# Performance work log

Measured on AMD Instinct MI355X. Metric: run time of the kernel, lower is better.

## Reference

```python
import jax, jax.numpy as jnp
import numpy as np

OUT, IN, GROUP, RANK, NPROT, BATCH = 4096, 4096, 128, 32, 32, 4096


def setup_inputs() -> dict:
    key = jax.random.key(0)
    k = jax.random.split(key, 7)
    n = OUT * IN
    x = jax.random.normal(k[0], (BATCH, IN), dtype=jnp.float32)
    # two int4 values per byte; byte values in [0,256)
    packed_int4 = jax.random.randint(k[1], (n // 2,), 0, 256, dtype=jnp.int32)
    # positive per-group scales (typical int4 scale magnitudes)
    scales = jax.random.uniform(k[2], (IN // GROUP,), dtype=jnp.float32, minval=0.005, maxval=0.02)
    svd_u = jax.random.normal(k[3], (OUT, RANK), dtype=jnp.float32) * 0.01
    svd_v = jax.random.normal(k[4], (IN, RANK), dtype=jnp.float32) * 0.01
    protected_channels = jax.random.normal(k[5], (NPROT, IN), dtype=jnp.float32) * 0.02
    # unique protected row indices
    protected_indices = jax.random.permutation(k[6], OUT)[:NPROT].astype(jnp.int32)
    return {
        "x": x,
        "packed_int4": packed_int4,
        "scales": scales,
        "svd_u": svd_u,
        "svd_v": svd_v,
        "protected_channels": protected_channels,
        "protected_indices": protected_indices,
    }


def reference(x, packed_int4, scales, svd_u, svd_v, protected_channels, protected_indices):
    out_f = svd_u.shape[0]
    in_f = x.shape[-1]
    group = in_f // scales.shape[0]
    # Unpack: original puts low nibbles in first half of the flat array,
    # high nibbles in the second half (split layout, not interleaved).
    lo = packed_int4 & 15
    hi = (packed_int4 >> 4) & 15
    unpacked = jnp.concatenate([lo, hi])  # [out*in]
    w_quant = (unpacked.astype(jnp.float32) - 8.0).reshape(out_f, in_f)
    # per-group dequant over input columns
    w = (w_quant.reshape(out_f, -1, group) * scales[None, :, None]).reshape(out_f, in_f)
    # low-rank SVD correction
    w = w + svd_u @ svd_v.T
    # protected output channels overwrite full rows
    w = w.at[protected_indices].set(protected_channels)
    out = x @ w.T  # [batch, out]
    return out.astype(jnp.float16)
```

## Files before the change

kernel.cpp:

```cpp
#include <hip/hip_runtime.h>
#include <hip/hip_bf16.h>
#include <hip/hip_fp16.h>

#define OUT_F 4096
#define IN_F  4096
#define BATCH 4096
#define RANK  32
#define KPAD  4160
#define NKB   130
#define NT    65

typedef __hip_bfloat16 bf16;
using bf16x8 = __attribute__((ext_vector_type(8))) short;
using f32x4  = __attribute__((ext_vector_type(4))) float;


__device__ __forceinline__ void gload_lds16(const void* g, void* l) {
  __builtin_amdgcn_global_load_lds(
      (const __attribute__((address_space(1))) unsigned int*)g,
      (__attribute__((address_space(3))) unsigned int*)l,
      16, 0, 0);
}

__device__ __forceinline__ unsigned short bf16_bits(float f) {
  bf16 h = __float2bfloat16(f);
  return *(unsigned short*)&h;
}

#define SBAR() asm volatile("s_barrier" ::: "memory")

__global__ __launch_bounds__(256) void prep_misc(const float* __restrict__ v,
                                                 const float* __restrict__ scales,
                                                 const float* __restrict__ u,
                                                 const int* __restrict__ pidx,
                                                 bf16* __restrict__ vst,
                                                 bf16* __restrict__ B) {
  int bid = blockIdx.x;
  if (bid < 512) {
    int gid = bid * 256 + threadIdx.x;
    int c = gid >> 5, r = gid & 31;
    float val = v[(size_t)c * RANK + r] / scales[c >> 7];
    vst[(size_t)r * IN_F + c] = __float2bfloat16(val);
  } else {
    int i = (bid - 512) * 256 + threadIdx.x;
    int o = i >> 6, j = i & 63;
    float val = (j < RANK) ? u[o * RANK + j] : 0.f;
#pragma unroll
    for (int jj = 0; jj < 32; ++jj)
      if (pidx[jj] == o) val = 0.f;
    B[(size_t)o * KPAD + IN_F + j] = __float2bfloat16(val);
  }
}

__global__ __launch_bounds__(512) void prep_a(const float* __restrict__ x,
                                              const float* __restrict__ scales,
                                              const bf16* __restrict__ vst,
                                              bf16* __restrict__ A) {
  __shared__ __align__(16) char lds[16384];
  int rb = blockIdx.x;
  int tid = threadIdx.x, w = tid >> 6, l = tid & 63;

  for (int c = 0; c < 8; ++c) {
#pragma unroll
    for (int j = 0; j < 2; ++j) {
      int r = w * 2 + j;
      const float* xr = x + (size_t)(rb * 16 + r) * IN_F + c * 512 + l * 8;
      float sv = scales[(c * 512 + l * 8) >> 7];
      float4 v0 = *(const float4*)xr;
      float4 v1 = *(const float4*)(xr + 4);
      bf16x8 pk;
      pk[0] = (short)bf16_bits(v0.x * sv); pk[1] = (short)bf16_bits(v0.y * sv);
      pk[2] = (short)bf16_bits(v0.z * sv); pk[3] = (short)bf16_bits(v0.w * sv);
      pk[4] = (short)bf16_bits(v1.x * sv); pk[5] = (short)bf16_bits(v1.y * sv);
      pk[6] = (short)bf16_bits(v1.z * sv); pk[7] = (short)bf16_bits(v1.w * sv);
      int kb = l >> 2;
      int byte = kb * 1024 + (((l & 3) << 4) + r) * 16;
      *(bf16x8*)(lds + (byte ^ ((kb & 7) << 4))) = pk;
    }
    __syncthreads();
#pragma unroll
    for (int j = 0; j < 2; ++j) {
      int f = w * 2 + j;
      int byte = f * 1024 + l * 16;
      bf16x8 pk = *(const bf16x8*)(lds + (byte ^ ((f & 7) << 4)));
      *(bf16x8*)(A + ((size_t)rb * NKB + c * 16 + f) * 512 + (size_t)l * 8) = pk;
    }
    __syncthreads();
  }

  const bf16* abase = A + (size_t)rb * NKB * 512 + (size_t)l * 8;
  const bf16* brow0 = vst + (size_t)(l & 15) * IN_F + ((l >> 4) << 3);
  const bf16* brow1 = vst + (size_t)(16 + (l & 15)) * IN_F + ((l >> 4) << 3);
  f32x4 acc0 = (f32x4){0.f, 0.f, 0.f, 0.f};
  f32x4 acc1 = (f32x4){0.f, 0.f, 0.f, 0.f};
#pragma unroll 8
  for (int k32 = w * 16; k32 < w * 16 + 16; ++k32) {
    bf16x8 av  = *(const bf16x8*)(abase + (size_t)k32 * 512);
    bf16x8 bv0 = *(const bf16x8*)(brow0 + k32 * 32);
    bf16x8 bv1 = *(const bf16x8*)(brow1 + k32 * 32);
    acc0 = __builtin_amdgcn_mfma_f32_16x16x32_bf16(av, bv0, acc0, 0, 0, 0);
    acc1 = __builtin_amdgcn_mfma_f32_16x16x32_bf16(av, bv1, acc1, 0, 0, 0);
  }
  *(f32x4*)(lds + w * 2048 + l * 32)      = acc0;
  *(f32x4*)(lds + w * 2048 + l * 32 + 16) = acc1;
  __syncthreads();
  if (w == 1) {
    bf16x8 z = (bf16x8){0, 0, 0, 0, 0, 0, 0, 0};
    *(bf16x8*)(A + ((size_t)rb * NKB + 129) * 512 + (size_t)l * 8) = z;
  }
  if (w == 0) {
#pragma unroll
    for (int ww = 1; ww < 8; ++ww) {
      acc0 += *(const f32x4*)(lds + ww * 2048 + l * 32);
      acc1 += *(const f32x4*)(lds + ww * 2048 + l * 32 + 16);
    }
    bf16* base = A + ((size_t)rb * NKB + 128) * 512;
    int c0 = l & 15, c1 = 16 + (l & 15);
#pragma unroll
    for (int r = 0; r < 4; ++r) {
      int row15 = ((l >> 4) << 2) + r;
      base[(c0 >> 3) * 128 + row15 * 8 + (c0 & 7)] = __float2bfloat16(acc0[r]);
      base[(c1 >> 3) * 128 + row15 * 8 + (c1 & 7)] = __float2bfloat16(acc1[r]);
    }
  }
}

__global__ __launch_bounds__(256) void prep_b(const int* __restrict__ packed,
                                              const float* __restrict__ pc,
                                              const float* __restrict__ scales,
                                              const int* __restrict__ pidx,
                                              bf16* __restrict__ B) {
  size_t i = (size_t)blockIdx.x * 256 + threadIdx.x;
  int4 p = ((const int4*)packed)[i];
  size_t e = i * 4;
  int o = (int)(e >> 12);
  int c = (int)(e & 4095);
  int pi_lo = -1, pi_hi = -1;
#pragma unroll
  for (int j = 0; j < 32; ++j) {
    int pr = pidx[j];
    if (pr == o) pi_lo = j;
    if (pr == o + 2048) pi_hi = j;
  }
  int vals[4] = {p.x, p.y, p.z, p.w};
  unsigned short lo[4], hi[4];
#pragma unroll
  for (int j = 0; j < 4; ++j) {
    lo[j] = bf16_bits((float)((vals[j] & 15) - 8));
    hi[j] = bf16_bits((float)(((vals[j] >> 4) & 15) - 8));
  }
  if (pi_lo >= 0) {
    float sv = scales[c >> 7];
#pragma unroll
    for (int j = 0; j < 4; ++j)
      lo[j] = bf16_bits(pc[(size_t)pi_lo * IN_F + c + j] / sv);
  }
  if (pi_hi >= 0) {
    float sv = scales[c >> 7];
#pragma unroll
    for (int j = 0; j < 4; ++j)
      hi[j] = bf16_bits(pc[(size_t)pi_hi * IN_F + c + j] / sv);
  }
  *(ushort4*)(B + (size_t)o * KPAD + c) = make_ushort4(lo[0], lo[1], lo[2], lo[3]);
  *(ushort4*)(B + (size_t)(o + 2048) * KPAD + c) = make_ushort4(hi[0], hi[1], hi[2], hi[3]);
}

__global__ __launch_bounds__(512, 2) void gemm_bt(const bf16* __restrict__ A,
                                                  const bf16* __restrict__ B,
                                                  float* __restrict__ out) {
  __shared__ __align__(16) bf16 Bs[4 * 256 * 64];

  int bid = blockIdx.x;
  int swz = (bid & 7) * 32 + (bid >> 3);
  int brow = (swz >> 4) << 8;
  int bcol = (swz & 15) << 8;

  int tid = threadIdx.x;
  int lane = tid & 63;
  int wave = tid >> 6;
  int wr = wave >> 1;
  int wc = wave & 1;

  f32x4 acc[4][8];
#pragma unroll
  for (int m = 0; m < 4; ++m)
#pragma unroll
    for (int n = 0; n < 8; ++n)
      acc[m][n] = (f32x4){0.f, 0.f, 0.f, 0.f};

  const char* abase[4];
  int rbw = (brow >> 4) + wr * 4;
#pragma unroll
  for (int m = 0; m < 4; ++m)
    abase[m] = (const char*)A + ((size_t)(rbw + m) * NKB) * 1024 + lane * 16;

  int boff[8];
#pragma unroll
  for (int n = 0; n < 8; ++n) {
    int rbr = wc * 128 + n * 16 + (lane & 15);
    int s0 = (lane >> 4) ^ (rbr & 7);
    boff[n] = rbr * 128 + (s0 << 4);
  }

  const bf16* gB[4]; int lB[4];
#pragma unroll
  for (int q = 0; q < 4; ++q) {
    int idx = q * 512 + tid;
    int row = idx >> 3, slot = idx & 7;
    gB[q] = B + (size_t)(bcol + row) * KPAD + ((slot ^ (row & 7)) << 3);
    lB[q] = idx << 4;
  }
  char* bs0 = (char*)Bs;

  bf16x8 a0[4][2], a1[4][2];
#pragma unroll
  for (int m = 0; m < 4; ++m)
#pragma unroll
    for (int kk = 0; kk < 2; ++kk)
      a0[m][kk] = *(const bf16x8*)(abase[m] + kk * 1024);
#pragma unroll
  for (int kt = 0; kt < 3; ++kt)
#pragma unroll
    for (int q = 0; q < 4; ++q)
      gload_lds16(gB[q] + kt * 64, bs0 + kt * 32768 + lB[q]);
  asm volatile("s_waitcnt vmcnt(8)" ::: "memory");
  SBAR();

  auto tile_body = [&](int t, bf16x8 (&Au)[4][2], bf16x8 (&Ap)[4][2], bool pref) {
    const char* rb_ = bs0 + (t & 3) * 32768;
    char* wb = bs0 + ((t + 3) & 3) * 32768;
    int kt = (t + 3 < NT) ? (t + 3) : (NT - 1);
#pragma unroll
    for (int p = 0; p < 4; ++p) {
      if (p == 0 && pref) {
#pragma unroll
        for (int m = 0; m < 4; ++m)
#pragma unroll
          for (int kk = 0; kk < 2; ++kk)
            Ap[m][kk] = *(const bf16x8*)(abase[m] + (size_t)(2 * (t + 1) + kk) * 1024);
      }
      bf16x8 bv0k0 = *(const bf16x8*)(rb_ + boff[2 * p]);
      bf16x8 bv0k1 = *(const bf16x8*)(rb_ + (boff[2 * p] ^ 64));
      bf16x8 bv1k0 = *(const bf16x8*)(rb_ + boff[2 * p + 1]);
      bf16x8 bv1k1 = *(const bf16x8*)(rb_ + (boff[2 * p + 1] ^ 64));
      gload_lds16(gB[p] + (size_t)kt * 64, wb + lB[p]);
      __builtin_amdgcn_s_setprio(1);
#pragma unroll
      for (int m = 0; m < 4; ++m) {
        acc[m][2 * p]     = __builtin_amdgcn_mfma_f32_16x16x32_bf16(Au[m][0], bv0k0, acc[m][2 * p], 0, 0, 0);
        acc[m][2 * p]     = __builtin_amdgcn_mfma_f32_16x16x32_bf16(Au[m][1], bv0k1, acc[m][2 * p], 0, 0, 0);
        acc[m][2 * p + 1] = __builtin_amdgcn_mfma_f32_16x16x32_bf16(Au[m][0], bv1k0, acc[m][2 * p + 1], 0, 0, 0);
        acc[m][2 * p + 1] = __builtin_amdgcn_mfma_f32_16x16x32_bf16(Au[m][1], bv1k1, acc[m][2 * p + 1], 0, 0, 0);
      }
      __builtin_amdgcn_s_setprio(0);
    }
    asm volatile("s_waitcnt vmcnt(4)" ::: "memory");
    SBAR();
  };

  for (int t = 0; t < NT - 1; t += 2) {
    tile_body(t, a0, a1, true);
    tile_body(t + 1, a1, a0, true);
  }
  tile_body(NT - 1, a0, a1, false);

#pragma unroll
  for (int m = 0; m < 4; ++m)
#pragma unroll
    for (int n = 0; n < 8; ++n)
#pragma unroll
      for (int r = 0; r < 4; ++r) {
        int mm = brow + wr * 64 + m * 16 + ((lane >> 4) << 2) + r;
        int nn = bcol + wc * 128 + n * 16 + (lane & 15);
        out[(size_t)mm * OUT_F + nn] = __half2float(__float2half(acc[m][n][r]));
      }
  asm volatile("s_waitcnt vmcnt(0)" ::: "memory");
}

extern "C" void kernel_launch(void* const* d_in, const int* in_sizes, int n_in,
                              void* d_out, int out_size, void* d_ws, size_t ws_size,
                              hipStream_t stream) {
  const float* x      = (const float*)d_in[0];
  const int*   packed = (const int*)d_in[1];
  const float* scales = (const float*)d_in[2];
  const float* svd_u  = (const float*)d_in[3];
  const float* svd_v  = (const float*)d_in[4];
  const float* pc     = (const float*)d_in[5];
  const int*   pidx   = (const int*)d_in[6];
  float* out = (float*)d_out;

  bf16* A   = (bf16*)d_ws;
  bf16* B   = A + (size_t)BATCH * KPAD;
  bf16* vst = B + (size_t)OUT_F * KPAD;

  prep_misc<<<1536, 256, 0, stream>>>(svd_v, scales, svd_u, pidx, vst, B);
  prep_a   <<<256,  512, 0, stream>>>(x, scales, vst, A);
  prep_b   <<<8192, 256, 0, stream>>>(packed, pc, scales, pidx, B);
  gemm_bt  <<<256,  512, 0, stream>>>(A, B, out);
}
```

Measured before the change: 289.5 us.

## Halve GEMM N-tile to 128, double grid and occupancy, drop A double-buffering

Shrinks the per-block output tile from 256x256 to 256x128, doubling the grid to 512 blocks and raising launch bounds to 4 blocks per CU with half the LDS buffer. The A-fragment register double-buffer is replaced by a single buffer reloaded at the end of each k-tile, before the barrier. This is meant to raise occupancy and wave-level parallelism to hide latency. In exchange it lowers data reuse per block, doubles total A reads, and exposes A global-load latency on each iteration.

Measured after the change: 299.3 us. 3.4% more time.

```diff
diff --git a/kernel.cpp b/kernel.cpp
--- a/kernel.cpp
+++ b/kernel.cpp
@@ -165,15 +165,15 @@
   *(ushort4*)(B + (size_t)(o + 2048) * KPAD + c) = make_ushort4(hi[0], hi[1], hi[2], hi[3]);
 }
 
-__global__ __launch_bounds__(512, 2) void gemm_bt(const bf16* __restrict__ A,
+__global__ __launch_bounds__(512, 4) void gemm_bt(const bf16* __restrict__ A,
                                                   const bf16* __restrict__ B,
                                                   float* __restrict__ out) {
-  __shared__ __align__(16) bf16 Bs[4 * 256 * 64];
+  __shared__ __align__(16) bf16 Bs[4 * 128 * 64];
 
   int bid = blockIdx.x;
-  int swz = (bid & 7) * 32 + (bid >> 3);
-  int brow = (swz >> 4) << 8;
-  int bcol = (swz & 15) << 8;
+  int swz = (bid & 7) * 64 + (bid >> 3);
+  int brow = (swz >> 5) << 8;
+  int bcol = (swz & 31) << 7;
 
   int tid = threadIdx.x;
   int lane = tid & 63;
@@ -181,30 +181,31 @@
   int wr = wave >> 1;
   int wc = wave & 1;
 
-  f32x4 acc[4][8];
-#pragma unroll
-  for (int m = 0; m < 4; ++m)
-#pragma unroll
-    for (int n = 0; n < 8; ++n)
+  f32x4 acc[4][4];
+#pragma unroll
+  for (int m = 0; m < 4; ++m)
+#pragma unroll
+    for (int n = 0; n < 4; ++n)
       acc[m][n] = (f32x4){0.f, 0.f, 0.f, 0.f};
 
-  const char* abase[4];
+  unsigned aoff[4];
   int rbw = (brow >> 4) + wr * 4;
 #pragma unroll
   for (int m = 0; m < 4; ++m)
-    abase[m] = (const char*)A + ((size_t)(rbw + m) * NKB) * 1024 + lane * 16;
-
-  int boff[8];
-#pragma unroll
-  for (int n = 0; n < 8; ++n) {
-    int rbr = wc * 128 + n * 16 + (lane & 15);
+    aoff[m] = (unsigned)((rbw + m) * NKB) * 1024u + (unsigned)lane * 16u;
+  const char* Ab = (const char*)A;
+
+  int boff[4];
+#pragma unroll
+  for (int n = 0; n < 4; ++n) {
+    int rbr = wc * 64 + n * 16 + (lane & 15);
     int s0 = (lane >> 4) ^ (rbr & 7);
     boff[n] = rbr * 128 + (s0 << 4);
   }
 
-  const bf16* gB[4]; int lB[4];
-#pragma unroll
-  for (int q = 0; q < 4; ++q) {
+  const bf16* gB[2]; int lB[2];
+#pragma unroll
+  for (int q = 0; q < 2; ++q) {
     int idx = q * 512 + tid;
     int row = idx >> 3, slot = idx & 7;
     gB[q] = B + (size_t)(bcol + row) * KPAD + ((slot ^ (row & 7)) << 3);
@@ -212,66 +213,58 @@
   }
   char* bs0 = (char*)Bs;
 
-  bf16x8 a0[4][2], a1[4][2];
+  bf16x8 a[4][2];
 #pragma unroll
   for (int m = 0; m < 4; ++m)
 #pragma unroll
     for (int kk = 0; kk < 2; ++kk)
-      a0[m][kk] = *(const bf16x8*)(abase[m] + kk * 1024);
+      a[m][kk] = *(const bf16x8*)(Ab + aoff[m] + kk * 1024);
 #pragma unroll
   for (int kt = 0; kt < 3; ++kt)
 #pragma unroll
-    for (int q = 0; q < 4; ++q)
-      gload_lds16(gB[q] + kt * 64, bs0 + kt * 32768 + lB[q]);
-  asm volatile("s_waitcnt vmcnt(8)" ::: "memory");
+    for (int q = 0; q < 2; ++q)
+      gload_lds16(gB[q] + kt * 64, bs0 + kt * 16384 + lB[q]);
+  asm volatile("s_waitcnt vmcnt(4)" ::: "memory");
   SBAR();
 
-  auto tile_body = [&](int t, bf16x8 (&Au)[4][2], bf16x8 (&Ap)[4][2], bool pref) {
-    const char* rb_ = bs0 + (t & 3) * 32768;
-    char* wb = bs0 + ((t + 3) & 3) * 32768;
+  for (int t = 0; t < NT; ++t) {
+    const char* rb_ = bs0 + (t & 3) * 16384;
+    char* wb = bs0 + ((t + 3) & 3) * 16384;
     int kt = (t + 3 < NT) ? (t + 3) : (NT - 1);
 #pragma unroll
     for (int p = 0; p < 4; ++p) {
-      if (p == 0 && pref) {
-#pragma unroll
-        for (int m = 0; m < 4; ++m)
-#pragma unroll
-          for (int kk = 0; kk < 2; ++kk)
-            Ap[m][kk] = *(const bf16x8*)(abase[m] + (size_t)(2 * (t + 1) + kk) * 1024);
-      }
-      bf16x8 bv0k0 = *(const bf16x8*)(rb_ + boff[2 * p]);
-      bf16x8 bv0k1 = *(const bf16x8*)(rb_ + (boff[2 * p] ^ 64));
-      bf16x8 bv1k0 = *(const bf16x8*)(rb_ + boff[2 * p + 1]);
-      bf16x8 bv1k1 = *(const bf16x8*)(rb_ + (boff[2 * p + 1] ^ 64));
-      gload_lds16(gB[p] + (size_t)kt * 64, wb + lB[p]);
+      bf16x8 bv0 = *(const bf16x8*)(rb_ + boff[p]);
+      bf16x8 bv1 = *(const bf16x8*)(rb_ + (boff[p] ^ 64));
+      if (p == 1) gload_lds16(gB[0] + (size_t)kt * 64, wb + lB[0]);
+      if (p == 3) gload_lds16(gB[1] + (size_t)kt * 64, wb + lB[1]);
       __builtin_amdgcn_s_setprio(1);
 #pragma unroll
       for (int m = 0; m < 4; ++m) {
-        acc[m][2 * p]     = __builtin_amdgcn_mfma_f32_16x16x32_bf16(Au[m][0], bv0k0, acc[m][2 * p], 0, 0, 0);
-        acc[m][2 * p]     = __builtin_amdgcn_mfma_f32_16x16x32_bf16(Au[m][1], bv0k1, acc[m][2 * p], 0, 0, 0);
-        acc[m][2 * p + 1] = __builtin_amdgcn_mfma_f32_16x16x32_bf16(Au[m][0], bv1k0, acc[m][2 * p + 1], 0, 0, 0);
-        acc[m][2 * p + 1] = __builtin_amdgcn_mfma_f32_16x16x32_bf16(Au[m][1], bv1k1, acc[m][2 * p + 1], 0, 0, 0);
+        acc[m][p] = __builtin_amdgcn_mfma_f32_16x16x32_bf16(a[m][0], bv0, acc[m][p], 0, 0, 0);
+        acc[m][p] = __builtin_amdgcn_mfma_f32_16x16x32_bf16(a[m][1], bv1, acc[m][p], 0, 0, 0);
       }
       __builtin_amdgcn_s_setprio(0);
     }
-    asm volatile("s_waitcnt vmcnt(4)" ::: "memory");
+    asm volatile("s_waitcnt vmcnt(2)" ::: "memory");
+    if (t + 1 < NT) {
+      unsigned ko = (unsigned)(2 * (t + 1)) * 1024u;
+#pragma unroll
+      for (int m = 0; m < 4; ++m)
+#pragma unroll
+        for (int kk = 0; kk < 2; ++kk)
+          a[m][kk] = *(const bf16x8*)(Ab + aoff[m] + ko + kk * 1024);
+    }
     SBAR();
-  };
-
-  for (int t = 0; t < NT - 1; t += 2) {
-    tile_body(t, a0, a1, true);
-    tile_body(t + 1, a1, a0, true);
-  }
-  tile_body(NT - 1, a0, a1, false);
-
-#pragma unroll
-  for (int m = 0; m < 4; ++m)
-#pragma unroll
-    for (int n = 0; n < 8; ++n)
+  }
+
+#pragma unroll
+  for (int m = 0; m < 4; ++m)
+#pragma unroll
+    for (int n = 0; n < 4; ++n)
 #pragma unroll
       for (int r = 0; r < 4; ++r) {
         int mm = brow + wr * 64 + m * 16 + ((lane >> 4) << 2) + r;
-        int nn = bcol + wc * 128 + n * 16 + (lane & 15);
+        int nn = bcol + wc * 64 + n * 16 + (lane & 15);
         out[(size_t)mm * OUT_F + nn] = __half2float(__float2half(acc[m][n][r]));
       }
   asm volatile("s_waitcnt vmcnt(0)" ::: "memory");
@@ -296,5 +289,5 @@
   prep_misc<<<1536, 256, 0, stream>>>(svd_v, scales, svd_u, pidx, vst, B);
   prep_a   <<<256,  512, 0, stream>>>(x, scales, vst, A);
   prep_b   <<<8192, 256, 0, stream>>>(packed, pc, scales, pidx, B);
-  gemm_bt  <<<256,  512, 0, stream>>>(A, B, out);
-}
+  gemm_bt  <<<512,  512, 0, stream>>>(A, B, out);
+}
```
